# Optimization experiments

Measured on AMD Instinct MI355X. Metric: run time of the kernel, lower is better.

## Reference

```python
import jax, jax.numpy as jnp
import numpy as np

D_MODEL = 512
N_EXPERTS = 8
TOPK = 2
D_FF = D_MODEL * 4
LB_WEIGHT = 0.01


def setup_inputs() -> dict:
    key = jax.random.key(0)
    k_x, k_g, k_w1, k_v1, k_w2 = jax.random.split(key, 5)
    B, L = 4, 2048
    x = jax.random.normal(k_x, (B, L, D_MODEL), dtype=jnp.float32)
    # nn.Linear gate weight, init std=0.01, shape [n_experts, d_model]
    gate_w = 0.01 * jax.random.normal(k_g, (N_EXPERTS, D_MODEL), dtype=jnp.float32)
    # kaiming_normal_ fan_in / relu: std = sqrt(2 / fan_in); fan_in is last dim
    std1 = np.sqrt(2.0 / D_MODEL).astype(np.float32)
    std2 = np.sqrt(2.0 / D_FF).astype(np.float32)
    W1 = std1 * jax.random.normal(k_w1, (N_EXPERTS, D_FF, D_MODEL), dtype=jnp.float32)
    V1 = std1 * jax.random.normal(k_v1, (N_EXPERTS, D_FF, D_MODEL), dtype=jnp.float32)
    W2 = std2 * jax.random.normal(k_w2, (N_EXPERTS, D_MODEL, D_FF), dtype=jnp.float32)
    return {"x": x, "gate_w": gate_w, "W1": W1, "V1": V1, "W2": W2}


def reference(x, gate_w, W1, V1, W2):
    B, L, D = x.shape
    T = B * L
    x_flat = x.reshape(T, D)

    # --- gating ---
    logits = x_flat @ gate_w.T                      # [T, E]
    probs = jax.nn.softmax(logits, axis=-1)         # [T, E]
    scores, indices = jax.lax.top_k(probs, TOPK)    # [T, K] each

    # combine weights: [T, E]; top-k indices per token are distinct
    oh = jax.nn.one_hot(indices, N_EXPERTS, dtype=x.dtype)    # [T, K, E]
    combine = jnp.einsum('tke,tk->te', oh, scores)            # [T, E]

    # load-balancing aux loss
    load = oh.sum(axis=(0, 1))                      # [E] tokens routed per expert
    f = load / T
    P = probs.mean(axis=0)                          # [E]
    aux_loss = N_EXPERTS * jnp.sum(f * P) * LB_WEIGHT

    # --- SwiGLU experts (dense over experts, masked combine) ---
    h = jnp.einsum('td,efd->etf', x_flat, W1)       # [E, T, d_ff]
    v = jnp.einsum('td,efd->etf', x_flat, V1)       # [E, T, d_ff]
    y = jnp.einsum('etf,edf->etd', jax.nn.silu(h) * v, W2)   # [E, T, D]

    out = jnp.einsum('te,etd->td', combine, y).reshape(B, L, D)
    return out, aux_loss
```

## Files before the change

kernel.cpp:

```cpp
#include <hip/hip_runtime.h>
#include <hip/hip_bf16.h>
#include <stdint.h>

#define D_MODEL 512
#define N_EXP 8
#define D_FF 2048
#define NTOK 8192
#define TM 256
#define MAX_TILES 72
#define NEPAD (MAX_TILES*TM)
#define BK 64

typedef __attribute__((ext_vector_type(8))) short short8;
typedef __attribute__((ext_vector_type(4))) float f32x4;

struct Ctrl {
  int cnt[8];
  int cursor[8];
  int offpad[16];
  int ntiles;
  int pad[3];
  int texp[MAX_TILES];
};

__device__ __forceinline__ unsigned short f2bf(float f){
  unsigned u = __float_as_uint(f);
  u += 0x7FFFu + ((u>>16)&1u);
  return (unsigned short)(u>>16);
}
__device__ __forceinline__ float bf2f(unsigned short v){
  return __uint_as_float(((unsigned)v)<<16);
}

__device__ __forceinline__ short8 pack8(float4 a, float4 b){
  short8 o;
  o[0]=(short)f2bf(a.x); o[1]=(short)f2bf(a.y); o[2]=(short)f2bf(a.z); o[3]=(short)f2bf(a.w);
  o[4]=(short)f2bf(b.x); o[5]=(short)f2bf(b.y); o[6]=(short)f2bf(b.z); o[7]=(short)f2bf(b.w);
  return o;
}

__device__ __forceinline__ void gload16(const void* g, void* l){
  __builtin_amdgcn_global_load_lds((const __attribute__((address_space(1))) unsigned int*)g,
                                   (__attribute__((address_space(3))) unsigned int*)l, 16, 0, 0);
}

#define SBAR0 __builtin_amdgcn_sched_barrier(0)
#define BAR   do{ SBAR0; __builtin_amdgcn_s_barrier(); SBAR0; }while(0)
#define LGKM0 do{ asm volatile("s_waitcnt lgkmcnt(0)" ::: "memory"); SBAR0; }while(0)
#define VM(N) do{ asm volatile("s_waitcnt vmcnt(" #N ")" ::: "memory"); SBAR0; }while(0)

__global__ void __launch_bounds__(256)
prep_kernel(const float* __restrict__ x, const float* __restrict__ gw,
            const float* __restrict__ W1, const float* __restrict__ V1, const float* __restrict__ W2,
            unsigned short* __restrict__ W1b, unsigned short* __restrict__ V1b, unsigned short* __restrict__ W2d,
            int* __restrict__ tok_e, float* __restrict__ tok_s,
            Ctrl* __restrict__ c, float* __restrict__ Pbins,
            unsigned short* __restrict__ Xb){
  __shared__ float gws[N_EXP*D_MODEL];
  __shared__ float pblk[4][8];
  __shared__ int cblk[8];
  int bid = blockIdx.x;
  int tid = threadIdx.x;
  if(bid >= 2048){
    int j = bid - 2048;
    const float* src = (j<4096) ? W1 : (j<8192 ? V1 : W2);
    unsigned short* dst = (j<4096) ? W1b : (j<8192 ? V1b : W2d);
    int i = (j & 4095)*2048 + tid*8;
    float4 a = *(const float4*)(src+i);
    float4 b = *(const float4*)(src+i+4);
    *(short8*)(dst+i) = pack8(a,b);
    return;
  }
  for(int i=tid; i<N_EXP*D_MODEL; i+=256) gws[i]=gw[i];
  if(tid<8) cblk[tid]=0;
  __syncthreads();
  int wave = tid>>6, lane = tid&63;
  int t = bid*4 + wave;
  const float* xr = x + (size_t)t*D_MODEL + lane*8;
  float4 xa = *(const float4*)xr;
  float4 xb = *(const float4*)(xr+4);
  *(short8*)(Xb + (size_t)t*D_MODEL + lane*8) = pack8(xa,xb);
  float le[8];
  #pragma unroll
  for(int e=0;e<8;e++){
    const float* g = gws + e*D_MODEL + lane*8;
    float4 ga = *(const float4*)g;
    float4 gb = *(const float4*)(g+4);
    le[e] = xa.x*ga.x + xa.y*ga.y + xa.z*ga.z + xa.w*ga.w
          + xb.x*gb.x + xb.y*gb.y + xb.z*gb.z + xb.w*gb.w;
  }
  #pragma unroll
  for(int e=0;e<8;e++){
    float v = le[e];
    #pragma unroll
    for(int off=1; off<64; off<<=1) v += __shfl_xor(v, off);
    le[e]=v;
  }
  float mx = le[0];
  #pragma unroll
  for(int e=1;e<8;e++) mx = fmaxf(mx, le[e]);
  float p[8], s=0.f;
  #pragma unroll
  for(int e=0;e<8;e++){ p[e]=__expf(le[e]-mx); s+=p[e]; }
  float inv = 1.0f/s;
  #pragma unroll
  for(int e=0;e<8;e++) p[e]*=inv;
  int e0=0; float s0=p[0];
  #pragma unroll
  for(int e=1;e<8;e++) if(p[e]>s0){e0=e;s0=p[e];}
  int e1=-1; float s1=-1.f;
  #pragma unroll
  for(int e=0;e<8;e++) if(e!=e0 && p[e]>s1){e1=e;s1=p[e];}
  if(lane==0){
    tok_e[2*t]=e0; tok_e[2*t+1]=e1;
    tok_s[2*t]=s0; tok_s[2*t+1]=s1;
    atomicAdd(&cblk[e0],1); atomicAdd(&cblk[e1],1);
    #pragma unroll
    for(int e=0;e<8;e++) pblk[wave][e]=p[e];
  }
  __syncthreads();
  if(tid<8){
    atomicAdd(&c->cnt[tid], cblk[tid]);
    atomicAdd(&Pbins[(bid&63)*8 + tid],
              pblk[0][tid]+pblk[1][tid]+pblk[2][tid]+pblk[3][tid]);
  }
}

__global__ void __launch_bounds__(256)
cvt_kernel(const float* __restrict__ src, unsigned short* __restrict__ dst, int n){
  int i = (blockIdx.x*256 + threadIdx.x)*8;
  if(i >= n) return;
  float4 a = *(const float4*)(src+i);
  float4 b = *(const float4*)(src+i+4);
  *(short8*)(dst+i) = pack8(a,b);
}

__global__ void __launch_bounds__(256)
scatter_kernel(const int* __restrict__ tok_e, const float* __restrict__ tok_s,
               Ctrl* __restrict__ c, int* __restrict__ etok, float* __restrict__ escl,
               int* __restrict__ pos, const float* __restrict__ Pbins, float* __restrict__ out){
  __shared__ int soff[8];
  __shared__ float pred[4][8];
  int tid = threadIdx.x;
  if(tid==0){
    int o=0;
    #pragma unroll
    for(int e=0;e<8;e++){ soff[e]=o; o += ((c->cnt[e]+TM-1)/TM)*TM; }
  }
  __syncthreads();
  int t = blockIdx.x*256 + tid;
  #pragma unroll
  for(int k=0;k<2;k++){
    int e = tok_e[2*t+k];
    int p = atomicAdd(&c->cursor[e],1);
    int i = soff[e]+p;
    etok[i]=t; escl[i]=tok_s[2*t+k];
    pos[2*t+k]=i;
  }
  if(blockIdx.x==0){
    float v = Pbins[tid] + Pbins[tid+256];
    v += __shfl_xor(v, 8);
    v += __shfl_xor(v, 16);
    v += __shfl_xor(v, 32);
    if((tid&63)<8) pred[tid>>6][tid&7] = v;
    __syncthreads();
    if(tid==0){
      int o=0, tc=0;
      float aux=0.f;
      #pragma unroll
      for(int e=0;e<8;e++){
        float tot = pred[0][e]+pred[1][e]+pred[2][e]+pred[3][e];
        c->offpad[e]=o;
        int nt = (c->cnt[e]+TM-1)/TM;
        for(int i=0;i<nt;i++) c->texp[tc++]=e;
        o += nt*TM;
        aux += ((float)c->cnt[e]/(float)NTOK) * (tot/(float)NTOK);
      }
      c->offpad[8]=o;
      c->ntiles=tc;
      out[(size_t)NTOK*D_MODEL] = 8.0f*0.01f*aux;
    }
  }
}

__global__ void __launch_bounds__(512,2)
expA_kernel(const unsigned short* __restrict__ Xb, const unsigned short* __restrict__ W1b,
            const unsigned short* __restrict__ V1b, const int* __restrict__ etok,
            const Ctrl* __restrict__ c, unsigned short* __restrict__ G){
  __shared__ short8 As[2][2048];
  __shared__ short8 Bs[2][2048];
  int bid = blockIdx.x;
  int chunk = bid & 7;
  int w_in = bid >> 3;
  int fb = w_in / 9;
  int tile = chunk*9 + (w_in - fb*9);
  int fbase = fb * 128;
  if(tile >= c->ntiles) return;
  int e = c->texp[tile];
  int base = tile*TM;
  int tid = threadIdx.x;

  int r0 = tid>>3;
  int cs = (tid&7) ^ (r0&7);
  int t0 = etok[base + r0] & (NTOK-1);
  int t1 = etok[base + 64 + r0] & (NTOK-1);
  int t2 = etok[base + 128 + r0] & (NTOK-1);
  int t3 = etok[base + 192 + r0] & (NTOK-1);
  const unsigned short* sA0 = Xb + (size_t)t0*D_MODEL + cs*8;
  const unsigned short* sA1 = Xb + (size_t)t1*D_MODEL + cs*8;
  const unsigned short* sA2 = Xb + (size_t)t2*D_MODEL + cs*8;
  const unsigned short* sA3 = Xb + (size_t)t3*D_MODEL + cs*8;
  const unsigned short* WE = W1b + (size_t)e*(D_FF*D_MODEL);
  const unsigned short* VE = V1b + (size_t)e*(D_FF*D_MODEL);
  const unsigned short* sB0 = WE + (size_t)(fbase+r0)*D_MODEL + cs*8;
  const unsigned short* sB1 = WE + (size_t)(fbase+64+r0)*D_MODEL + cs*8;
  const unsigned short* sB2 = VE + (size_t)(fbase+r0)*D_MODEL + cs*8;
  const unsigned short* sB3 = VE + (size_t)(fbase+64+r0)*D_MODEL + cs*8;
  int w64 = tid & ~63;

  int lane = tid&63, lrow = lane&15, lk = lane>>4;
  int wid = tid>>6, wr = wid>>2, wc = wid&3;
  int sw = lrow&7;
  int ch0 = lk ^ sw;
  int ch1 = (4+lk) ^ sw;

  f32x4 hacc[8][2], vacc[8][2];
  #pragma unroll
  for(int mi=0;mi<8;mi++)
    #pragma unroll
    for(int nj=0;nj<2;nj++){
      hacc[mi][nj]=(f32x4){0.f,0.f,0.f,0.f};
      vacc[mi][nj]=(f32x4){0.f,0.f,0.f,0.f};
    }

  auto ST_ALL = [&](int b, int kt){
    size_t o=(size_t)kt*BK;
    gload16(sA0+o, &As[b][w64]);      gload16(sA1+o, &As[b][512+w64]);
    gload16(sA2+o, &As[b][1024+w64]); gload16(sA3+o, &As[b][1536+w64]);
    gload16(sB0+o, &Bs[b][w64]);      gload16(sB1+o, &Bs[b][512+w64]);
    gload16(sB2+o, &Bs[b][1024+w64]); gload16(sB3+o, &Bs[b][1536+w64]);
  };

  ST_ALL(0,0);
  ST_ALL(1,1);
  VM(8);
  BAR;

  short8 alo[4][2], ahi[4][2], bw[2][2], bv[2][2];

  #pragma unroll
  for(int k=0;k<8;k++){
    const int cur = k&1;
    #pragma unroll
    for(int j=0;j<4;j++){
      int s = (wr*128 + j*16 + lrow)*8;
      alo[j][0] = As[cur][s + ch0];
      alo[j][1] = As[cur][s + ch1];
    }
    #pragma unroll
    for(int nj=0;nj<2;nj++){
      int s = (wc*32 + nj*16 + lrow)*8;
      bw[nj][0] = Bs[cur][s + ch0];
      bw[nj][1] = Bs[cur][s + ch1];
    }
    __builtin_amdgcn_s_setprio(1);
    #pragma unroll
    for(int j=0;j<4;j++)
      #pragma unroll
      for(int nj=0;nj<2;nj++){
        hacc[j][nj] = __builtin_amdgcn_mfma_f32_16x16x32_bf16(alo[j][0], bw[nj][0], hacc[j][nj],0,0,0);
        hacc[j][nj] = __builtin_amdgcn_mfma_f32_16x16x32_bf16(alo[j][1], bw[nj][1], hacc[j][nj],0,0,0);
      }
    __builtin_amdgcn_s_setprio(0);
    #pragma unroll
    for(int nj=0;nj<2;nj++){
      int s = 1024 + (wc*32 + nj*16 + lrow)*8;
      bv[nj][0] = Bs[cur][s + ch0];
      bv[nj][1] = Bs[cur][s + ch1];
    }
    __builtin_amdgcn_s_setprio(1);
    #pragma unroll
    for(int j=0;j<4;j++)
      #pragma unroll
      for(int nj=0;nj<2;nj++){
        vacc[j][nj] = __builtin_amdgcn_mfma_f32_16x16x32_bf16(alo[j][0], bv[nj][0], vacc[j][nj],0,0,0);
        vacc[j][nj] = __builtin_amdgcn_mfma_f32_16x16x32_bf16(alo[j][1], bv[nj][1], vacc[j][nj],0,0,0);
      }
    __builtin_amdgcn_s_setprio(0);
    #pragma unroll
    for(int j=0;j<4;j++){
      int s = (wr*128 + 64 + j*16 + lrow)*8;
      ahi[j][0] = As[cur][s + ch0];
      ahi[j][1] = As[cur][s + ch1];
    }
    __builtin_amdgcn_s_setprio(1);
    #pragma unroll
    for(int j=0;j<4;j++)
      #pragma unroll
      for(int nj=0;nj<2;nj++){
        vacc[4+j][nj] = __builtin_amdgcn_mfma_f32_16x16x32_bf16(ahi[j][0], bv[nj][0], vacc[4+j][nj],0,0,0);
        vacc[4+j][nj] = __builtin_amdgcn_mfma_f32_16x16x32_bf16(ahi[j][1], bv[nj][1], vacc[4+j][nj],0,0,0);
      }
    __builtin_amdgcn_s_setprio(0);
    LGKM0;
    BAR;
    if(k<6) ST_ALL(cur, k+2);
    __builtin_amdgcn_s_setprio(1);
    #pragma unroll
    for(int j=0;j<4;j++)
      #pragma unroll
      for(int nj=0;nj<2;nj++){
        hacc[4+j][nj] = __builtin_amdgcn_mfma_f32_16x16x32_bf16(ahi[j][0], bw[nj][0], hacc[4+j][nj],0,0,0);
        hacc[4+j][nj] = __builtin_amdgcn_mfma_f32_16x16x32_bf16(ahi[j][1], bw[nj][1], hacc[4+j][nj],0,0,0);
      }
    __builtin_amdgcn_s_setprio(0);
    if(k<6){ VM(8); } else if(k==6){ VM(0); }
    BAR;
  }

  #pragma unroll
  for(int mi=0;mi<8;mi++){
    int m = base + wr*128 + mi*16 + lk*4;
    #pragma unroll
    for(int nj=0;nj<2;nj++){
      int f = fbase + wc*32 + nj*16 + lrow;
      #pragma unroll
      for(int r=0;r<4;r++){
        float h = hacc[mi][nj][r], vv = vacc[mi][nj][r];
        float g = (h/(1.0f+__expf(-h)))*vv;
        G[(size_t)(m+r)*D_FF + f] = f2bf(g);
      }
    }
  }
}

__global__ void __launch_bounds__(256,2)
expB_kernel(const unsigned short* __restrict__ G, const unsigned short* __restrict__ W2b,
            const Ctrl* __restrict__ c, unsigned short* __restrict__ Ye){
  __shared__ short8 As2[2][1024];
  __shared__ short8 Bs2[2][1024];
  int bid = blockIdx.x;
  int chunk = bid & 7;
  int w = bid >> 3;
  int nb = w / 18;
  int mt = chunk*18 + (w - nb*18);
  if(mt >= (c->offpad[8] >> 7)) return;
  int e = c->texp[mt>>1];
  int base = mt*128;
  int nbase = nb*128;
  int tid = threadIdx.x;

  int r0 = tid>>3;
  int cs = (tid&7) ^ (r0&7);
  const unsigned short* sA0 = G + (size_t)(base+r0)*D_FF + cs*8;
  const unsigned short* sA1 = G + (size_t)(base+32+r0)*D_FF + cs*8;
  const unsigned short* sA2 = G + (size_t)(base+64+r0)*D_FF + cs*8;
  const unsigned short* sA3 = G + (size_t)(base+96+r0)*D_FF + cs*8;
  const unsigned short* W2E = W2b + (size_t)e*(D_MODEL*D_FF);
  const unsigned short* sB0 = W2E + (size_t)(nbase+r0)*D_FF + cs*8;
  const unsigned short* sB1 = W2E + (size_t)(nbase+32+r0)*D_FF + cs*8;
  const unsigned short* sB2 = W2E + (size_t)(nbase+64+r0)*D_FF + cs*8;
  const unsigned short* sB3 = W2E + (size_t)(nbase+96+r0)*D_FF + cs*8;
  int w64 = tid & ~63;

  int lane = tid&63, lrow = lane&15, lk = lane>>4;
  int wid = tid>>6, wm = wid>>1, wn = wid&1;
  int sw = lrow&7;
  int ch0 = lk ^ sw;
  int ch1 = (4+lk) ^ sw;

  f32x4 acc[4][4];
  #pragma unroll
  for(int mi=0;mi<4;mi++)
    #pragma unroll
    for(int nj=0;nj<4;nj++) acc[mi][nj]=(f32x4){0.f,0.f,0.f,0.f};

  auto ST_ALL = [&](int b, int kt){
    size_t o=(size_t)kt*BK;
    gload16(sA0+o, &As2[b][w64]);      gload16(sA1+o, &As2[b][256+w64]);
    gload16(sA2+o, &As2[b][512+w64]);  gload16(sA3+o, &As2[b][768+w64]);
    gload16(sB0+o, &Bs2[b][w64]);      gload16(sB1+o, &Bs2[b][256+w64]);
    gload16(sB2+o, &Bs2[b][512+w64]);  gload16(sB3+o, &Bs2[b][768+w64]);
  };

  ST_ALL(0,0);
  ST_ALL(1,1);
  VM(8);
  BAR;

  short8 a[4][2], b[4][2];

  #pragma unroll 2
  for(int k=0;k<32;k++){
    const int cur = k&1;
    #pragma unroll
    for(int j=0;j<2;j++){
      int s = (wm*64 + j*16 + lrow)*8;
      a[j][0] = As2[cur][s + ch0];
      a[j][1] = As2[cur][s + ch1];
    }
    #pragma unroll
    for(int nj=0;nj<2;nj++){
      int s = (wn*64 + nj*16 + lrow)*8;
      b[nj][0] = Bs2[cur][s + ch0];
      b[nj][1] = Bs2[cur][s + ch1];
    }
    __builtin_amdgcn_s_setprio(1);
    #pragma unroll
    for(int j=0;j<2;j++)
      #pragma unroll
      for(int nj=0;nj<2;nj++){
        acc[j][nj] = __builtin_amdgcn_mfma_f32_16x16x32_bf16(a[j][0], b[nj][0], acc[j][nj],0,0,0);
        acc[j][nj] = __builtin_amdgcn_mfma_f32_16x16x32_bf16(a[j][1], b[nj][1], acc[j][nj],0,0,0);
      }
    __builtin_amdgcn_s_setprio(0);
    #pragma unroll
    for(int nj=0;nj<2;nj++){
      int s = (wn*64 + 32 + nj*16 + lrow)*8;
      b[2+nj][0] = Bs2[cur][s + ch0];
      b[2+nj][1] = Bs2[cur][s + ch1];
    }
    __builtin_amdgcn_s_setprio(1);
    #pragma unroll
    for(int j=0;j<2;j++)
      #pragma unroll
      for(int nj=0;nj<2;nj++){
        acc[j][2+nj] = __builtin_amdgcn_mfma_f32_16x16x32_bf16(a[j][0], b[2+nj][0], acc[j][2+nj],0,0,0);
        acc[j][2+nj] = __builtin_amdgcn_mfma_f32_16x16x32_bf16(a[j][1], b[2+nj][1], acc[j][2+nj],0,0,0);
      }
    __builtin_amdgcn_s_setprio(0);
    #pragma unroll
    for(int j=0;j<2;j++){
      int s = (wm*64 + 32 + j*16 + lrow)*8;
      a[2+j][0] = As2[cur][s + ch0];
      a[2+j][1] = As2[cur][s + ch1];
    }
    __builtin_amdgcn_s_setprio(1);
    #pragma unroll
    for(int j=0;j<2;j++)
      #pragma unroll
      for(int nj=0;nj<2;nj++){
        acc[2+j][2+nj] = __builtin_amdgcn_mfma_f32_16x16x32_bf16(a[2+j][0], b[2+nj][0], acc[2+j][2+nj],0,0,0);
        acc[2+j][2+nj] = __builtin_amdgcn_mfma_f32_16x16x32_bf16(a[2+j][1], b[2+nj][1], acc[2+j][2+nj],0,0,0);
      }
    __builtin_amdgcn_s_setprio(0);
    LGKM0;
    BAR;
    if(k<30) ST_ALL(cur, k+2);
    __builtin_amdgcn_s_setprio(1);
    #pragma unroll
    for(int j=0;j<2;j++)
      #pragma unroll
      for(int nj=0;nj<2;nj++){
        acc[2+j][nj] = __builtin_amdgcn_mfma_f32_16x16x32_bf16(a[2+j][0], b[nj][0], acc[2+j][nj],0,0,0);
        acc[2+j][nj] = __builtin_amdgcn_mfma_f32_16x16x32_bf16(a[2+j][1], b[nj][1], acc[2+j][nj],0,0,0);
      }
    __builtin_amdgcn_s_setprio(0);
    if(k<30){ VM(8); } else if(k==30){ VM(0); }
    BAR;
  }

  #pragma unroll
  for(int mi=0;mi<4;mi++){
    #pragma unroll
    for(int r=0;r<4;r++){
      int m = base + wm*64 + mi*16 + lk*4 + r;
      #pragma unroll
      for(int nj=0;nj<4;nj++){
        int n = nbase + wn*64 + nj*16 + lrow;
        Ye[(size_t)m*D_MODEL + n] = f2bf(acc[mi][nj][r]);
      }
    }
  }
}

__global__ void __launch_bounds__(256)
combine_kernel(const unsigned short* __restrict__ Ye, const int* __restrict__ pos,
               const float* __restrict__ tok_s, float* __restrict__ out){
  int wave = threadIdx.x>>6, lane = threadIdx.x&63;
  int t = blockIdx.x*4 + wave;
  int p0 = pos[2*t], p1 = pos[2*t+1];
  float s0 = tok_s[2*t], s1 = tok_s[2*t+1];
  short8 y0 = *(const short8*)(Ye + (size_t)p0*D_MODEL + lane*8);
  short8 y1 = *(const short8*)(Ye + (size_t)p1*D_MODEL + lane*8);
  float* o = out + (size_t)t*D_MODEL + lane*8;
  float v[8];
  #pragma unroll
  for(int i=0;i<8;i++)
    v[i] = s0*bf2f((unsigned short)y0[i]) + s1*bf2f((unsigned short)y1[i]);
  float4 lo = {v[0],v[1],v[2],v[3]};
  float4 hi = {v[4],v[5],v[6],v[7]};
  *(float4*)o = lo;
  *(float4*)(o+4) = hi;
}

extern "C" void kernel_launch(void* const* d_in, const int* in_sizes, int n_in,
                              void* d_out, int out_size, void* d_ws, size_t ws_size,
                              hipStream_t stream) {
  (void)in_sizes; (void)n_in; (void)out_size;
  const float* x  = (const float*)d_in[0];
  const float* gw = (const float*)d_in[1];
  const float* W1 = (const float*)d_in[2];
  const float* V1 = (const float*)d_in[3];
  const float* W2 = (const float*)d_in[4];
  float* out = (float*)d_out;

  const size_t WSZ = (size_t)N_EXP*D_FF*D_MODEL;
  const size_t XSZ = (size_t)NTOK*D_MODEL;
  char* ws = (char*)d_ws;
  size_t off = 0;
  unsigned short* W1b = (unsigned short*)(ws+off); off += WSZ*2;
  unsigned short* V1b = (unsigned short*)(ws+off); size_t v1_off = off; off += WSZ*2;
  unsigned short* Xb  = (unsigned short*)(ws+off); off += XSZ*2;
  unsigned short* G   = (unsigned short*)(ws+off); off += (size_t)NEPAD*D_FF*2;
  int*   etok  = (int*)(ws+off);   off += (size_t)NEPAD*4;
  float* escl  = (float*)(ws+off); off += (size_t)NEPAD*4;
  int*   pos   = (int*)(ws+off);   off += (size_t)NTOK*2*4;
  int*   tok_e = (int*)(ws+off);   off += (size_t)NTOK*2*4;
  float* tok_s = (float*)(ws+off); off += (size_t)NTOK*2*4;
  float* Pbins = (float*)(ws+off); size_t pb_off = off; off += 512*4;
  Ctrl*  ctrl  = (Ctrl*)(ws+off);  off += sizeof(Ctrl);
  size_t pb_bytes = off - pb_off;
  unsigned short* Ye  = (unsigned short*)(ws+v1_off);
  if(ws_size < off) return;

  unsigned short* W2d = (unsigned short*)(ws+off);
  bool hoistW2 = (ws_size >= off + WSZ*2);
  unsigned short* W2b = hoistW2 ? W2d : W1b;

  hipMemsetAsync(ws+pb_off, 0, pb_bytes, stream);

  int nconv = hoistW2 ? 3 : 2;
  prep_kernel<<<2048 + nconv*4096, 256, 0, stream>>>(x, gw, W1, V1, W2, W1b, V1b, W2d,
                                                     tok_e, tok_s, ctrl, Pbins, Xb);
  scatter_kernel<<<NTOK/256, 256, 0, stream>>>(tok_e, tok_s, ctrl, etok, escl, pos, Pbins, out);

  expA_kernel<<<1152, 512, 0, stream>>>(Xb, W1b, V1b, etok, ctrl, G);
  if(!hoistW2)
    cvt_kernel<<<(int)WSZ/(256*8), 256, 0, stream>>>(W2, W1b, (int)WSZ);
  expB_kernel<<<576, 256, 0, stream>>>(G, W2b, ctrl, Ye);
  combine_kernel<<<NTOK/4, 256, 0, stream>>>(Ye, pos, tok_s, out);
}
```

Measured before the change: 282.2 us.

## Split-K the second expert GEMM into two partial outputs summed in combine

The down-projection kernel now splits the D_FF reduction into two halves, doubling the grid from 576 to 1152 blocks. Each half writes its own bf16 partial result buffer, and the combine kernel reads and adds both partials when the W2 hoist path is active. The goal is better occupancy and load balance across CUs for a grid that was too small. The cost is extra partial-output traffic, an extra bf16 rounding of each partial, and reuse of the W1b region as scratch.

```diff
diff --git a/kernel.cpp b/kernel.cpp
--- a/kernel.cpp
+++ b/kernel.cpp
@@ -334,33 +334,38 @@
   }
 }
 
+template<int NSPLIT>
 __global__ void __launch_bounds__(256,2)
 expB_kernel(const unsigned short* __restrict__ G, const unsigned short* __restrict__ W2b,
             const Ctrl* __restrict__ c, unsigned short* __restrict__ Ye){
+  constexpr int KT = 32/NSPLIT;
   __shared__ short8 As2[2][1024];
   __shared__ short8 Bs2[2][1024];
   int bid = blockIdx.x;
   int chunk = bid & 7;
   int w = bid >> 3;
-  int nb = w / 18;
-  int mt = chunk*18 + (w - nb*18);
+  int ks = w / 72;
+  int r  = w - ks*72;
+  int nb = r / 18;
+  int mt = chunk*18 + (r - nb*18);
   if(mt >= (c->offpad[8] >> 7)) return;
   int e = c->texp[mt>>1];
   int base = mt*128;
   int nbase = nb*128;
+  int kbase = ks*KT*BK;
   int tid = threadIdx.x;
 
   int r0 = tid>>3;
   int cs = (tid&7) ^ (r0&7);
-  const unsigned short* sA0 = G + (size_t)(base+r0)*D_FF + cs*8;
-  const unsigned short* sA1 = G + (size_t)(base+32+r0)*D_FF + cs*8;
-  const unsigned short* sA2 = G + (size_t)(base+64+r0)*D_FF + cs*8;
-  const unsigned short* sA3 = G + (size_t)(base+96+r0)*D_FF + cs*8;
+  const unsigned short* sA0 = G + (size_t)(base+r0)*D_FF + kbase + cs*8;
+  const unsigned short* sA1 = G + (size_t)(base+32+r0)*D_FF + kbase + cs*8;
+  const unsigned short* sA2 = G + (size_t)(base+64+r0)*D_FF + kbase + cs*8;
+  const unsigned short* sA3 = G + (size_t)(base+96+r0)*D_FF + kbase + cs*8;
   const unsigned short* W2E = W2b + (size_t)e*(D_MODEL*D_FF);
-  const unsigned short* sB0 = W2E + (size_t)(nbase+r0)*D_FF + cs*8;
-  const unsigned short* sB1 = W2E + (size_t)(nbase+32+r0)*D_FF + cs*8;
-  const unsigned short* sB2 = W2E + (size_t)(nbase+64+r0)*D_FF + cs*8;
-  const unsigned short* sB3 = W2E + (size_t)(nbase+96+r0)*D_FF + cs*8;
+  const unsigned short* sB0 = W2E + (size_t)(nbase+r0)*D_FF + kbase + cs*8;
+  const unsigned short* sB1 = W2E + (size_t)(nbase+32+r0)*D_FF + kbase + cs*8;
+  const unsigned short* sB2 = W2E + (size_t)(nbase+64+r0)*D_FF + kbase + cs*8;
+  const unsigned short* sB3 = W2E + (size_t)(nbase+96+r0)*D_FF + kbase + cs*8;
   int w64 = tid & ~63;
 
   int lane = tid&63, lrow = lane&15, lk = lane>>4;
@@ -391,7 +396,7 @@
   short8 a[4][2], b[4][2];
 
   #pragma unroll 2
-  for(int k=0;k<32;k++){
+  for(int k=0;k<KT;k++){
     const int cur = k&1;
     #pragma unroll
     for(int j=0;j<2;j++){
@@ -446,7 +451,7 @@
     __builtin_amdgcn_s_setprio(0);
     LGKM0;
     BAR;
-    if(k<30) ST_ALL(cur, k+2);
+    if(k<KT-2) ST_ALL(cur, k+2);
     __builtin_amdgcn_s_setprio(1);
     #pragma unroll
     for(int j=0;j<2;j++)
@@ -456,19 +461,20 @@
         acc[2+j][nj] = __builtin_amdgcn_mfma_f32_16x16x32_bf16(a[2+j][1], b[nj][1], acc[2+j][nj],0,0,0);
       }
     __builtin_amdgcn_s_setprio(0);
-    if(k<30){ VM(8); } else if(k==30){ VM(0); }
+    if(k<KT-2){ VM(8); } else if(k==KT-2){ VM(0); }
     BAR;
   }
 
+  unsigned short* Yk = Ye + (size_t)ks*NEPAD*D_MODEL;
   #pragma unroll
   for(int mi=0;mi<4;mi++){
     #pragma unroll
-    for(int r=0;r<4;r++){
-      int m = base + wm*64 + mi*16 + lk*4 + r;
+    for(int r2=0;r2<4;r2++){
+      int m = base + wm*64 + mi*16 + lk*4 + r2;
       #pragma unroll
       for(int nj=0;nj<4;nj++){
         int n = nbase + wn*64 + nj*16 + lrow;
-        Ye[(size_t)m*D_MODEL + n] = f2bf(acc[mi][nj][r]);
+        Yk[(size_t)m*D_MODEL + n] = f2bf(acc[mi][nj][r2]);
       }
     }
   }
@@ -476,18 +482,26 @@
 
 __global__ void __launch_bounds__(256)
 combine_kernel(const unsigned short* __restrict__ Ye, const int* __restrict__ pos,
-               const float* __restrict__ tok_s, float* __restrict__ out){
+               const float* __restrict__ tok_s, float* __restrict__ out, int nsplit){
   int wave = threadIdx.x>>6, lane = threadIdx.x&63;
   int t = blockIdx.x*4 + wave;
   int p0 = pos[2*t], p1 = pos[2*t+1];
   float s0 = tok_s[2*t], s1 = tok_s[2*t+1];
   short8 y0 = *(const short8*)(Ye + (size_t)p0*D_MODEL + lane*8);
   short8 y1 = *(const short8*)(Ye + (size_t)p1*D_MODEL + lane*8);
-  float* o = out + (size_t)t*D_MODEL + lane*8;
   float v[8];
   #pragma unroll
   for(int i=0;i<8;i++)
     v[i] = s0*bf2f((unsigned short)y0[i]) + s1*bf2f((unsigned short)y1[i]);
+  if(nsplit==2){
+    const unsigned short* Y1 = Ye + (size_t)NEPAD*D_MODEL;
+    short8 z0 = *(const short8*)(Y1 + (size_t)p0*D_MODEL + lane*8);
+    short8 z1 = *(const short8*)(Y1 + (size_t)p1*D_MODEL + lane*8);
+    #pragma unroll
+    for(int i=0;i<8;i++)
+      v[i] += s0*bf2f((unsigned short)z0[i]) + s1*bf2f((unsigned short)z1[i]);
+  }
+  float* o = out + (size_t)t*D_MODEL + lane*8;
   float4 lo = {v[0],v[1],v[2],v[3]};
   float4 hi = {v[4],v[5],v[6],v[7]};
   *(float4*)o = lo;
@@ -521,12 +535,12 @@
   float* Pbins = (float*)(ws+off); size_t pb_off = off; off += 512*4;
   Ctrl*  ctrl  = (Ctrl*)(ws+off);  off += sizeof(Ctrl);
   size_t pb_bytes = off - pb_off;
-  unsigned short* Ye  = (unsigned short*)(ws+v1_off);
   if(ws_size < off) return;
 
   unsigned short* W2d = (unsigned short*)(ws+off);
   bool hoistW2 = (ws_size >= off + WSZ*2);
   unsigned short* W2b = hoistW2 ? W2d : W1b;
+  unsigned short* Ye  = hoistW2 ? (unsigned short*)ws : (unsigned short*)(ws+v1_off);
 
   hipMemsetAsync(ws+pb_off, 0, pb_bytes, stream);
 
@@ -538,6 +552,11 @@
   expA_kernel<<<1152, 512, 0, stream>>>(Xb, W1b, V1b, etok, ctrl, G);
   if(!hoistW2)
     cvt_kernel<<<(int)WSZ/(256*8), 256, 0, stream>>>(W2, W1b, (int)WSZ);
-  expB_kernel<<<576, 256, 0, stream>>>(G, W2b, ctrl, Ye);
-  combine_kernel<<<NTOK/4, 256, 0, stream>>>(Ye, pos, tok_s, out);
-}
+  if(hoistW2){
+    expB_kernel<2><<<1152, 256, 0, stream>>>(G, W2b, ctrl, Ye);
+    combine_kernel<<<NTOK/4, 256, 0, stream>>>(Ye, pos, tok_s, out, 2);
+  } else {
+    expB_kernel<1><<<576, 256, 0, stream>>>(G, W2b, ctrl, Ye);
+    combine_kernel<<<NTOK/4, 256, 0, stream>>>(Ye, pos, tok_s, out, 1);
+  }
+}
```

New measurement: 279.5 us. No clear change (-1.0%).
